# Kernel tuning notes

Measured on AMD Instinct MI355X. Metric: run time of the kernel, lower is better.

## Reference

```python
import jax, jax.numpy as jnp
import numpy as np

N, S, F, D = 4096, 128, 128, 256  # batch, memory slots, feat_dim, dim_h_o
EPS = 1e-8  # torch CosineSimilarity eps


def _xavier(key, shape):
    fan_out, fan_in = shape
    std = float(np.sqrt(2.0 / (fan_in + fan_out)))
    return jax.random.normal(key, shape, dtype=jnp.float32) * std


def setup_inputs() -> dict:
    key = jax.random.key(0)
    ks = jax.random.split(key, 10)
    return {
        "h_o_prev": jax.random.normal(ks[0], (N, D), dtype=jnp.float32),
        "C": jax.random.normal(ks[1], (N, S, F), dtype=jnp.float32),
        "Wk": _xavier(ks[2], (F, D)), "bk": jnp.zeros((F,), jnp.float32),
        "Wb": _xavier(ks[3], (1, D)), "bb": jnp.zeros((1,), jnp.float32),
        "We": _xavier(ks[4], (F, D)), "be": jnp.zeros((F,), jnp.float32),
        "Wv": _xavier(ks[5], (F, D)), "bv": jnp.zeros((F,), jnp.float32),
        "Wih": _xavier(ks[6], (3 * D, F)), "Whh": _xavier(ks[7], (3 * D, D)),
        "bih": jnp.zeros((3 * D,), jnp.float32), "bhh": jnp.zeros((3 * D,), jnp.float32),
    }


def reference(h_o_prev, C, Wk, bk, Wb, bb, We, be, Wv, bv, Wih, Whh, bih, bhh):
    # --- Attention (content addressing) ---
    k = h_o_prev @ Wk.T + bk                              # [N, F]
    beta_pre = h_o_prev @ Wb.T + bb                       # [N, 1]
    # clamp-split softplus trick in source == softplus(x) + 1
    beta = jax.nn.softplus(beta_pre) + 1.0                # [N, 1]
    C_norm = jnp.maximum(jnp.linalg.norm(C, axis=2), EPS)           # [N, S]
    k_norm = jnp.maximum(jnp.linalg.norm(k, axis=1, keepdims=True), EPS)  # [N, 1]
    s = jnp.einsum("nsf,nf->ns", C, k) / (C_norm * k_norm)          # cosine sim [N, S]
    w = jax.nn.softmax(s * beta, axis=1)                  # [N, S]
    # --- Read memory ---
    r = jnp.einsum("ns,nsf->nf", w, C)                    # [N, F]
    # --- GRU cell update (torch GRUCell semantics) ---
    gi = r @ Wih.T + bih                                  # [N, 3D]
    gh = h_o_prev @ Whh.T + bhh                           # [N, 3D]
    i_r, i_z, i_n = jnp.split(gi, 3, axis=1)
    h_r, h_z, h_n = jnp.split(gh, 3, axis=1)
    rg = jax.nn.sigmoid(i_r + h_r)
    z = jax.nn.sigmoid(i_z + h_z)
    n = jnp.tanh(i_n + rg * h_n)
    h_o = (1.0 - z) * n + z * h_o_prev                    # [N, D]
    # --- Write memory (erase + add, outer products) ---
    e = jax.nn.sigmoid(h_o @ We.T + be)                   # [N, F]
    v = h_o @ Wv.T + bv                                   # [N, F]
    w2 = w[:, :, None]                                    # [N, S, 1]
    C_new = C * (1.0 - w2 * e[:, None, :]) + w2 * v[:, None, :]
    return h_o, C_new, k, r
```

## Files before the change

### kernel.cpp

```cpp
#include <hip/hip_runtime.h>
#include <hip/hip_bf16.h>
#include <cstddef>
#include <cstdint>

constexpr int Nn = 4096;
constexpr int Ss = 128;
constexpr int Ff = 128;
constexpr int Dd = 256;
constexpr float EPSV = 1e-8f;

constexpr size_t HO_OFF = 0;
constexpr size_t C_OFF  = (size_t)Nn * Dd;
constexpr size_t K_OFF  = C_OFF + (size_t)Nn * Ss * Ff;
constexpr size_t R_OFF  = K_OFF + (size_t)Nn * Ff;

typedef __attribute__((ext_vector_type(4))) float f4v;
typedef __attribute__((ext_vector_type(8))) short bh8;

__device__ __forceinline__ float sigmf(float x) { return 1.0f / (1.0f + __expf(-x)); }

__device__ __forceinline__ short f2bf(float x) {
    __hip_bfloat16 h = __float2bfloat16(x);
    return *reinterpret_cast<short*>(&h);
}

template <int SIGSPLIT>
__global__ __launch_bounds__(256) void mfma_gemm(
    const float* __restrict__ A, int K,
    const float* __restrict__ W1, const float* __restrict__ W2, int splitW,
    const float* __restrict__ b1, const float* __restrict__ b2,
    float* __restrict__ out1, int J1,
    float* __restrict__ out2, int J2, int splitOut)
{
    __shared__ __align__(16) short sA[64 * 32];
    __shared__ __align__(16) short sW[64 * 32];

    const int t  = threadIdx.x;
    const int bm = blockIdx.x * 64;
    const int bj = blockIdx.y * 64;

    const int r  = t >> 2;
    const int kg = t & 3;
    const float* aRow = A + (size_t)(bm + r) * K;
    const int   colS  = bj + r;
    const float* wRow = (colS < splitW) ? (W1 + (size_t)colS * K)
                                        : (W2 + (size_t)(colS - splitW) * K);
    const int swzSt = r * 32 + ((kg ^ (r & 3)) << 3);

    const int l   = t & 63;
    const int wv  = t >> 6;
    const int wr  = wv >> 1;
    const int wc  = wv & 1;
    const int kgr = l >> 4;
    const int fr  = l & 15;

    f4v acc[2][2];
#pragma unroll
    for (int m = 0; m < 2; ++m)
#pragma unroll
        for (int n2 = 0; n2 < 2; ++n2) acc[m][n2] = f4v{0.f, 0.f, 0.f, 0.f};

    const int nk = K / 32;
    for (int kc = 0; kc < nk; ++kc) {
        const int k0 = kc * 32 + kg * 8;
        float4 a0 = *(const float4*)(aRow + k0);
        float4 a1 = *(const float4*)(aRow + k0 + 4);
        float4 w0 = *(const float4*)(wRow + k0);
        float4 w1 = *(const float4*)(wRow + k0 + 4);
        bh8 av = { f2bf(a0.x), f2bf(a0.y), f2bf(a0.z), f2bf(a0.w),
                   f2bf(a1.x), f2bf(a1.y), f2bf(a1.z), f2bf(a1.w) };
        bh8 wvv= { f2bf(w0.x), f2bf(w0.y), f2bf(w0.z), f2bf(w0.w),
                   f2bf(w1.x), f2bf(w1.y), f2bf(w1.z), f2bf(w1.w) };
        __syncthreads();
        *(bh8*)(sA + swzSt) = av;
        *(bh8*)(sW + swzSt) = wvv;
        __syncthreads();

        bh8 af[2], bf[2];
#pragma unroll
        for (int m = 0; m < 2; ++m) {
            int ar = wr * 32 + m * 16 + fr;
            af[m] = *(bh8*)(sA + ar * 32 + ((kgr ^ (ar & 3)) << 3));
            int bc = wc * 32 + m * 16 + fr;
            bf[m] = *(bh8*)(sW + bc * 32 + ((kgr ^ (bc & 3)) << 3));
        }
#pragma unroll
        for (int m = 0; m < 2; ++m)
#pragma unroll
            for (int n2 = 0; n2 < 2; ++n2)
                acc[m][n2] = __builtin_amdgcn_mfma_f32_16x16x32_bf16(
                    af[m], bf[n2], acc[m][n2], 0, 0, 0);
    }

#pragma unroll
    for (int n2 = 0; n2 < 2; ++n2) {
        const int colg = bj + wc * 32 + n2 * 16 + fr;
        const float bs = (colg < splitW) ? b1[colg] : b2[colg - splitW];
        float* base; int jj;
        if (colg < splitOut) { base = out1 + colg;              jj = J1; }
        else                 { base = out2 + (colg - splitOut); jj = J2; }
#pragma unroll
        for (int m = 0; m < 2; ++m) {
#pragma unroll
            for (int rg = 0; rg < 4; ++rg) {
                float x = acc[m][n2][rg] + bs;
                if (SIGSPLIT && colg < SIGSPLIT) x = sigmf(x);
                const int rowg = bm + wr * 32 + m * 16 + kgr * 4 + rg;
                base[(size_t)rowg * jj] = x;
            }
        }
    }
}

__global__ __launch_bounds__(256) void beta_kernel(
    const float* __restrict__ h, const float* __restrict__ Wb,
    const float* __restrict__ bb, float* __restrict__ beta_out)
{
    int wid  = threadIdx.x >> 6;
    int lane = threadIdx.x & 63;
    int n    = blockIdx.x * 4 + wid;
    float4 hv = *(const float4*)(h + (size_t)n * Dd + lane * 4);
    float4 wv = *(const float4*)(Wb + lane * 4);
    float p = hv.x * wv.x + hv.y * wv.y + hv.z * wv.z + hv.w * wv.w;
#pragma unroll
    for (int o = 32; o > 0; o >>= 1) p += __shfl_xor(p, o);
    if (lane == 0) {
        float bp = p + bb[0];
        float sp = (bp > 20.0f) ? bp : log1pf(__expf(bp));
        beta_out[n] = sp + 1.0f;
    }
}

__global__ __launch_bounds__(256) void attn_kernel(
    const float* __restrict__ C, const float* __restrict__ kvec,
    const float* __restrict__ beta_arr,
    float* __restrict__ w_out, float* __restrict__ r_out)
{
    const int n    = blockIdx.x;
    const int t    = threadIdx.x;
    const int lane = t & 63;
    const int wid  = t >> 6;
    const float* Cn = C + (size_t)n * Ss * Ff;

    __shared__ float sk[Ff];
    __shared__ float ssc[Ss];
    __shared__ float sred[8];
    __shared__ float sw[Ss];
    __shared__ float sr4[8][Ff];

    if (t < Ff) sk[t] = kvec[(size_t)n * Ff + t];
    __syncthreads();

    float ks = 0.0f;
    if (t < Ff) { float kv = sk[t]; ks = kv * kv; }
#pragma unroll
    for (int o = 32; o > 0; o >>= 1) ks += __shfl_xor(ks, o);
    if (lane == 0) sred[wid] = ks;
    __syncthreads();
    const float knorm = fmaxf(sqrtf(sred[0] + sred[1]), EPSV);
    const float beta  = beta_arr[n];

#pragma unroll 4
    for (int it = 0; it < 16; ++it) {
        int s = wid * 32 + it * 2 + (lane >> 5);
        int f = (lane & 31) * 4;
        float4 c4 = *(const float4*)(Cn + (size_t)s * Ff + f);
        float d = c4.x * sk[f] + c4.y * sk[f + 1] + c4.z * sk[f + 2] + c4.w * sk[f + 3];
        float q = c4.x * c4.x + c4.y * c4.y + c4.z * c4.z + c4.w * c4.w;
#pragma unroll
        for (int o = 16; o > 0; o >>= 1) {
            d += __shfl_xor(d, o);
            q += __shfl_xor(q, o);
        }
        if ((lane & 31) == 0) {
            float cn = fmaxf(sqrtf(q), EPSV);
            ssc[s] = d / (cn * knorm);
        }
    }
    __syncthreads();

    float x = -INFINITY;
    if (t < Ss) x = ssc[t] * beta;
    float m = x;
#pragma unroll
    for (int o = 32; o > 0; o >>= 1) m = fmaxf(m, __shfl_xor(m, o));
    if (lane == 0) sred[wid] = m;
    __syncthreads();
    const float gm = fmaxf(sred[0], sred[1]);
    float ex = (t < Ss) ? __expf(x - gm) : 0.0f;
    float sm = ex;
#pragma unroll
    for (int o = 32; o > 0; o >>= 1) sm += __shfl_xor(sm, o);
    if (lane == 0) sred[4 + wid] = sm;
    __syncthreads();
    const float tot = sred[4] + sred[5];
    if (t < Ss) {
        float wvl = ex / tot;
        sw[t] = wvl;
        w_out[(size_t)n * Ss + t] = wvl;
    }
    __syncthreads();

    const int f4 = (t & 31) * 4;
    const int sg = t >> 5;
    float4 racc = make_float4(0.f, 0.f, 0.f, 0.f);
#pragma unroll 4
    for (int j = 0; j < 16; ++j) {
        int s = sg * 16 + j;
        float wvl = sw[s];
        float4 c4 = *(const float4*)(Cn + (size_t)s * Ff + f4);
        racc.x += wvl * c4.x;
        racc.y += wvl * c4.y;
        racc.z += wvl * c4.z;
        racc.w += wvl * c4.w;
    }
    *(float4*)(&sr4[sg][f4]) = racc;
    __syncthreads();
    if (t < 32) {
        float4 rr = *(float4*)(&sr4[0][t * 4]);
#pragma unroll
        for (int g = 1; g < 8; ++g) {
            float4 p = *(float4*)(&sr4[g][t * 4]);
            rr.x += p.x; rr.y += p.y; rr.z += p.z; rr.w += p.w;
        }
        *(float4*)(r_out + (size_t)n * Ff + t * 4) = rr;
    }
}

__global__ __launch_bounds__(256) void gates_kernel(
    const float* __restrict__ gi, const float* __restrict__ gh,
    const float* __restrict__ hprev, float* __restrict__ ho)
{
    int idx = blockIdx.x * blockDim.x + threadIdx.x;
    int n  = idx >> 6;
    int d4 = (idx & 63) * 4;
    const float* gin = gi + (size_t)n * 768;
    const float* ghn = gh + (size_t)n * 768;
    float4 ir = *(const float4*)(gin + d4);
    float4 iz = *(const float4*)(gin + 256 + d4);
    float4 in_ = *(const float4*)(gin + 512 + d4);
    float4 hr = *(const float4*)(ghn + d4);
    float4 hz = *(const float4*)(ghn + 256 + d4);
    float4 hn = *(const float4*)(ghn + 512 + d4);
    float4 hp = *(const float4*)(hprev + (size_t)n * Dd + d4);
    float4 o;
    { float rg = sigmf(ir.x + hr.x); float z = sigmf(iz.x + hz.x);
      float nn = tanhf(in_.x + rg * hn.x); o.x = (1.0f - z) * nn + z * hp.x; }
    { float rg = sigmf(ir.y + hr.y); float z = sigmf(iz.y + hz.y);
      float nn = tanhf(in_.y + rg * hn.y); o.y = (1.0f - z) * nn + z * hp.y; }
    { float rg = sigmf(ir.z + hr.z); float z = sigmf(iz.z + hz.z);
      float nn = tanhf(in_.z + rg * hn.z); o.z = (1.0f - z) * nn + z * hp.z; }
    { float rg = sigmf(ir.w + hr.w); float z = sigmf(iz.w + hz.w);
      float nn = tanhf(in_.w + rg * hn.w); o.w = (1.0f - z) * nn + z * hp.w; }
    *(float4*)(ho + (size_t)n * Dd + d4) = o;
}

__global__ __launch_bounds__(256) void update_kernel(
    const float* __restrict__ C, const float* __restrict__ w,
    const float* __restrict__ ev, float* __restrict__ Cnew)
{
    const size_t total4 = (size_t)Nn * Ss * Ff / 4;
    const size_t stride = (size_t)gridDim.x * blockDim.x;
    const size_t lin    = (size_t)blockIdx.x * blockDim.x + threadIdx.x;
    const int nIter     = (int)(total4 / stride);
    for (int it = nIter - 1; it >= 0; --it) {
        size_t i = (size_t)it * stride + lin;
        int n   = (int)(i >> 12);
        int rem = (int)(i & 4095);
        int s   = rem >> 5;
        int f4  = (rem & 31) * 4;
        float wv = w[(size_t)n * Ss + s];
        float4 e4 = *(const float4*)(ev + (size_t)n * 256 + f4);
        float4 v4 = *(const float4*)(ev + (size_t)n * 256 + 128 + f4);
        f4v c4 = __builtin_nontemporal_load((const f4v*)(C + i * 4));
        f4v o;
        o.x = c4.x * (1.0f - wv * e4.x) + wv * v4.x;
        o.y = c4.y * (1.0f - wv * e4.y) + wv * v4.y;
        o.z = c4.z * (1.0f - wv * e4.z) + wv * v4.z;
        o.w = c4.w * (1.0f - wv * e4.w) + wv * v4.w;
        __builtin_nontemporal_store(o, (f4v*)(Cnew + i * 4));
    }
}

extern "C" void kernel_launch(void* const* d_in, const int* in_sizes, int n_in,
                              void* d_out, int out_size, void* d_ws, size_t ws_size,
                              hipStream_t stream)
{
    const float* h_prev = (const float*)d_in[0];
    const float* C      = (const float*)d_in[1];
    const float* Wk     = (const float*)d_in[2];
    const float* bk     = (const float*)d_in[3];
    const float* Wb     = (const float*)d_in[4];
    const float* bb     = (const float*)d_in[5];
    const float* We     = (const float*)d_in[6];
    const float* be     = (const float*)d_in[7];
    const float* Wv     = (const float*)d_in[8];
    const float* bv     = (const float*)d_in[9];
    const float* Wih    = (const float*)d_in[10];
    const float* Whh    = (const float*)d_in[11];
    const float* bih    = (const float*)d_in[12];
    const float* bhh    = (const float*)d_in[13];

    float* out  = (float*)d_out;
    float* ho   = out + HO_OFF;
    float* Cnew = out + C_OFF;
    float* kbuf = out + K_OFF;
    float* rbuf = out + R_OFF;

    float* ws      = (float*)d_ws;
    float* ws_gh   = ws;
    float* ws_gi   = ws_gh + (size_t)Nn * 768;
    float* ws_beta = ws_gi + (size_t)Nn * 768;
    float* ws_w    = ws_beta + Nn;
    float* ws_ev   = ws_w + (size_t)Nn * Ss;

    mfma_gemm<0><<<dim3(Nn / 64, 896 / 64), 256, 0, stream>>>(
        h_prev, Dd, Whh, Wk, 768, bhh, bk, ws_gh, 768, kbuf, 128, 768);

    beta_kernel<<<Nn / 4, 256, 0, stream>>>(h_prev, Wb, bb, ws_beta);

    attn_kernel<<<Nn, 256, 0, stream>>>(C, kbuf, ws_beta, ws_w, rbuf);

    mfma_gemm<0><<<dim3(Nn / 64, 768 / 64), 256, 0, stream>>>(
        rbuf, Ff, Wih, Wih, 768, bih, bih, ws_gi, 768, nullptr, 0, 768);

    gates_kernel<<<(Nn * Dd / 4) / 256, 256, 0, stream>>>(ws_gi, ws_gh, h_prev, ho);

    mfma_gemm<128><<<dim3(Nn / 64, 256 / 64), 256, 0, stream>>>(
        ho, Dd, We, Wv, 128, be, bv, ws_ev, 256, nullptr, 0, 256);

    update_kernel<<<8192, 256, 0, stream>>>(C, ws_w, ws_ev, Cnew);
}
```

Baseline: 227.8 us.

## Fuse whole memory-cell step into one per-batch-tile mega kernel

Replaces seven kernels with a weight-to-bf16 prep kernel and one fused kernel that handles 8 batch rows per block. Each block runs the key projection, the cosine attention with an online softmax, the GRU GEMMs and gates, and the erase/add GEMM and C update. Intermediates such as gi, gh, w and e/v stay in LDS, and C is read twice from the same block, which improves its chance of cache reuse. The cost is tiny MFMA tiles padded to 16 rows with only 8 used, fewer blocks in the grid, and heavy LDS use that may limit occupancy.

After: 191.0 us. 16.2% less time.

```diff
diff --git a/kernel.cpp b/kernel.cpp
--- a/kernel.cpp
+++ b/kernel.cpp
@@ -16,6 +16,13 @@
 
 typedef __attribute__((ext_vector_type(4))) float f4v;
 typedef __attribute__((ext_vector_type(8))) short bh8;
+typedef __attribute__((ext_vector_type(4))) short bh4;
+
+constexpr int WK_O  = 0;
+constexpr int WHH_O = 32768;
+constexpr int WIH_O = 229376;
+constexpr int WEV_O = 327680;
+constexpr int W_TOT = 393216;
 
 __device__ __forceinline__ float sigmf(float x) { return 1.0f / (1.0f + __expf(-x)); }
 
@@ -24,261 +31,248 @@
     return *reinterpret_cast<short*>(&h);
 }
 
-template <int SIGSPLIT>
-__global__ __launch_bounds__(256) void mfma_gemm(
-    const float* __restrict__ A, int K,
-    const float* __restrict__ W1, const float* __restrict__ W2, int splitW,
-    const float* __restrict__ b1, const float* __restrict__ b2,
-    float* __restrict__ out1, int J1,
-    float* __restrict__ out2, int J2, int splitOut)
+__device__ __forceinline__ int swzH(int row, int kb) { return row * 512 + (kb ^ ((row & 7) << 4)); }
+__device__ __forceinline__ int swzR(int row, int kb) { return row * 256 + (kb ^ ((row & 7) << 4)); }
+
+__device__ __forceinline__ f4v mfma16(bh8 a, bh8 b, f4v c) {
+    return __builtin_amdgcn_mfma_f32_16x16x32_bf16(a, b, c, 0, 0, 0);
+}
+
+__global__ __launch_bounds__(256) void prep_weights(
+    const float* __restrict__ Wk, const float* __restrict__ Whh,
+    const float* __restrict__ Wih, const float* __restrict__ We,
+    const float* __restrict__ Wv, short* __restrict__ out)
 {
-    __shared__ __align__(16) short sA[64 * 32];
-    __shared__ __align__(16) short sW[64 * 32];
+    int id = blockIdx.x * 256 + threadIdx.x;
+    float v;
+    if      (id < WHH_O) v = Wk[id - WK_O];
+    else if (id < WIH_O) v = Whh[id - WHH_O];
+    else if (id < WEV_O) v = Wih[id - WIH_O];
+    else if (id < WEV_O + 32768) v = We[id - WEV_O];
+    else v = Wv[id - WEV_O - 32768];
+    out[id] = f2bf(v);
+}
+
+__global__ __launch_bounds__(512, 4) void mega_kernel(
+    const float* __restrict__ C, const float* __restrict__ h_prev,
+    const short* __restrict__ WB,
+    const float* __restrict__ Wb, const float* __restrict__ bb,
+    const float* __restrict__ bk, const float* __restrict__ bhh,
+    const float* __restrict__ bih, const float* __restrict__ be,
+    const float* __restrict__ bv,
+    float* __restrict__ ho, float* __restrict__ Cnew,
+    float* __restrict__ kout, float* __restrict__ rout)
+{
+    __shared__ float sH[8][256];
+    __shared__ __align__(16) short sHb[16 * 256];
+    __shared__ __align__(16) short sRb[16 * 128];
+    __shared__ float sK[8][128];
+    __shared__ float sSc[8][128];
+    __shared__ float sGs[8][768];
+    __shared__ float sGn[8][256];
+    __shared__ float sEV[8][256];
 
     const int t  = threadIdx.x;
-    const int bm = blockIdx.x * 64;
-    const int bj = blockIdx.y * 64;
-
-    const int r  = t >> 2;
-    const int kg = t & 3;
-    const float* aRow = A + (size_t)(bm + r) * K;
-    const int   colS  = bj + r;
-    const float* wRow = (colS < splitW) ? (W1 + (size_t)colS * K)
-                                        : (W2 + (size_t)(colS - splitW) * K);
-    const int swzSt = r * 32 + ((kg ^ (r & 3)) << 3);
-
-    const int l   = t & 63;
-    const int wv  = t >> 6;
-    const int wr  = wv >> 1;
-    const int wc  = wv & 1;
-    const int kgr = l >> 4;
-    const int fr  = l & 15;
-
-    f4v acc[2][2];
-#pragma unroll
-    for (int m = 0; m < 2; ++m)
-#pragma unroll
-        for (int n2 = 0; n2 < 2; ++n2) acc[m][n2] = f4v{0.f, 0.f, 0.f, 0.f};
-
-    const int nk = K / 32;
-    for (int kc = 0; kc < nk; ++kc) {
-        const int k0 = kc * 32 + kg * 8;
-        float4 a0 = *(const float4*)(aRow + k0);
-        float4 a1 = *(const float4*)(aRow + k0 + 4);
-        float4 w0 = *(const float4*)(wRow + k0);
-        float4 w1 = *(const float4*)(wRow + k0 + 4);
-        bh8 av = { f2bf(a0.x), f2bf(a0.y), f2bf(a0.z), f2bf(a0.w),
-                   f2bf(a1.x), f2bf(a1.y), f2bf(a1.z), f2bf(a1.w) };
-        bh8 wvv= { f2bf(w0.x), f2bf(w0.y), f2bf(w0.z), f2bf(w0.w),
-                   f2bf(w1.x), f2bf(w1.y), f2bf(w1.z), f2bf(w1.w) };
-        __syncthreads();
-        *(bh8*)(sA + swzSt) = av;
-        *(bh8*)(sW + swzSt) = wvv;
-        __syncthreads();
-
-        bh8 af[2], bf[2];
-#pragma unroll
-        for (int m = 0; m < 2; ++m) {
-            int ar = wr * 32 + m * 16 + fr;
-            af[m] = *(bh8*)(sA + ar * 32 + ((kgr ^ (ar & 3)) << 3));
-            int bc = wc * 32 + m * 16 + fr;
-            bf[m] = *(bh8*)(sW + bc * 32 + ((kgr ^ (bc & 3)) << 3));
-        }
-#pragma unroll
-        for (int m = 0; m < 2; ++m)
-#pragma unroll
-            for (int n2 = 0; n2 < 2; ++n2)
-                acc[m][n2] = __builtin_amdgcn_mfma_f32_16x16x32_bf16(
-                    af[m], bf[n2], acc[m][n2], 0, 0, 0);
-    }
-
-#pragma unroll
-    for (int n2 = 0; n2 < 2; ++n2) {
-        const int colg = bj + wc * 32 + n2 * 16 + fr;
-        const float bs = (colg < splitW) ? b1[colg] : b2[colg - splitW];
-        float* base; int jj;
-        if (colg < splitOut) { base = out1 + colg;              jj = J1; }
-        else                 { base = out2 + (colg - splitOut); jj = J2; }
-#pragma unroll
-        for (int m = 0; m < 2; ++m) {
+    const int l  = t & 63;
+    const int wv = t >> 6;
+    const int nb = blockIdx.x * 8;
+    char* hb = (char*)sHb;
+    char* rb = (char*)sRb;
+
+    const short* WkB  = WB + WK_O;
+    const short* WhhB = WB + WHH_O;
+    const short* WihB = WB + WIH_O;
+    const short* WevB = WB + WEV_O;
+
+    {
+        const int f = t * 4, row = f >> 8, col = f & 255;
+        float4 hv = *(const float4*)(h_prev + (size_t)(nb + row) * Dd + col);
+        *(float4*)&sH[row][col] = hv;
+        bh4 hb4 = { f2bf(hv.x), f2bf(hv.y), f2bf(hv.z), f2bf(hv.w) };
+        *(bh4*)(hb + swzH(row, col * 2)) = hb4;
+        *(int4*)(hb + 8192 + t * 16) = int4{0, 0, 0, 0};
+        *(int*)(rb + 2048 + t * 4) = 0;
+    }
+    __syncthreads();
+
+    {
+        const int fr = l & 15, kq = l >> 4, rbase = kq * 4;
+        const int colg = wv * 16 + fr;
+        f4v acc = {0.f, 0.f, 0.f, 0.f};
+#pragma unroll
+        for (int kc = 0; kc < 8; ++kc) {
+            bh8 a = *(const bh8*)(hb + swzH(fr, kc * 64 + kq * 16));
+            bh8 b = *(const bh8*)(WkB + (size_t)colg * 256 + kc * 32 + kq * 8);
+            acc = mfma16(a, b, acc);
+        }
+        if (rbase < 8) {
+            const float bs = bk[colg];
 #pragma unroll
             for (int rg = 0; rg < 4; ++rg) {
-                float x = acc[m][n2][rg] + bs;
-                if (SIGSPLIT && colg < SIGSPLIT) x = sigmf(x);
-                const int rowg = bm + wr * 32 + m * 16 + kgr * 4 + rg;
-                base[(size_t)rowg * jj] = x;
-            }
-        }
-    }
-}
-
-__global__ __launch_bounds__(256) void beta_kernel(
-    const float* __restrict__ h, const float* __restrict__ Wb,
-    const float* __restrict__ bb, float* __restrict__ beta_out)
-{
-    int wid  = threadIdx.x >> 6;
-    int lane = threadIdx.x & 63;
-    int n    = blockIdx.x * 4 + wid;
-    float4 hv = *(const float4*)(h + (size_t)n * Dd + lane * 4);
-    float4 wv = *(const float4*)(Wb + lane * 4);
-    float p = hv.x * wv.x + hv.y * wv.y + hv.z * wv.z + hv.w * wv.w;
-#pragma unroll
-    for (int o = 32; o > 0; o >>= 1) p += __shfl_xor(p, o);
-    if (lane == 0) {
-        float bp = p + bb[0];
-        float sp = (bp > 20.0f) ? bp : log1pf(__expf(bp));
-        beta_out[n] = sp + 1.0f;
-    }
-}
-
-__global__ __launch_bounds__(256) void attn_kernel(
-    const float* __restrict__ C, const float* __restrict__ kvec,
-    const float* __restrict__ beta_arr,
-    float* __restrict__ w_out, float* __restrict__ r_out)
-{
-    const int n    = blockIdx.x;
-    const int t    = threadIdx.x;
-    const int lane = t & 63;
-    const int wid  = t >> 6;
-    const float* Cn = C + (size_t)n * Ss * Ff;
-
-    __shared__ float sk[Ff];
-    __shared__ float ssc[Ss];
-    __shared__ float sred[8];
-    __shared__ float sw[Ss];
-    __shared__ float sr4[8][Ff];
-
-    if (t < Ff) sk[t] = kvec[(size_t)n * Ff + t];
-    __syncthreads();
-
-    float ks = 0.0f;
-    if (t < Ff) { float kv = sk[t]; ks = kv * kv; }
-#pragma unroll
-    for (int o = 32; o > 0; o >>= 1) ks += __shfl_xor(ks, o);
-    if (lane == 0) sred[wid] = ks;
-    __syncthreads();
-    const float knorm = fmaxf(sqrtf(sred[0] + sred[1]), EPSV);
-    const float beta  = beta_arr[n];
-
+                float x = acc[rg] + bs;
+                sK[rbase + rg][colg] = x;
+                kout[(size_t)(nb + rbase + rg) * Ff + colg] = x;
+            }
+        }
+    }
+    __syncthreads();
+
+    float M_r = 0.0f, invL_r = 0.0f;
+    {
+        const int half = l >> 5, fl = l & 31, f4 = fl * 4;
+        const float* Cn = C + (size_t)(nb + wv) * (Ss * Ff);
+
+        float kv0 = sK[wv][l], kv1 = sK[wv][64 + l];
+        float ks = kv0 * kv0 + kv1 * kv1;
+#pragma unroll
+        for (int o = 32; o > 0; o >>= 1) ks += __shfl_xor(ks, o);
+        const float knorm = fmaxf(sqrtf(ks), EPSV);
+
+        float4 hv = *(const float4*)&sH[wv][l * 4];
+        float4 wb4 = *(const float4*)(Wb + l * 4);
+        float bp = hv.x * wb4.x + hv.y * wb4.y + hv.z * wb4.z + hv.w * wb4.w;
+#pragma unroll
+        for (int o = 32; o > 0; o >>= 1) bp += __shfl_xor(bp, o);
+        bp += bb[0];
+        const float beta = ((bp > 20.0f) ? bp : log1pf(__expf(bp))) + 1.0f;
+
+        const float4 kreg = *(const float4*)&sK[wv][f4];
+        float m = -INFINITY, lsum = 0.0f;
+        f4v racc = {0.f, 0.f, 0.f, 0.f};
 #pragma unroll 4
-    for (int it = 0; it < 16; ++it) {
-        int s = wid * 32 + it * 2 + (lane >> 5);
-        int f = (lane & 31) * 4;
-        float4 c4 = *(const float4*)(Cn + (size_t)s * Ff + f);
-        float d = c4.x * sk[f] + c4.y * sk[f + 1] + c4.z * sk[f + 2] + c4.w * sk[f + 3];
-        float q = c4.x * c4.x + c4.y * c4.y + c4.z * c4.z + c4.w * c4.w;
-#pragma unroll
-        for (int o = 16; o > 0; o >>= 1) {
-            d += __shfl_xor(d, o);
-            q += __shfl_xor(q, o);
-        }
-        if ((lane & 31) == 0) {
-            float cn = fmaxf(sqrtf(q), EPSV);
-            ssc[s] = d / (cn * knorm);
-        }
-    }
-    __syncthreads();
-
-    float x = -INFINITY;
-    if (t < Ss) x = ssc[t] * beta;
-    float m = x;
-#pragma unroll
-    for (int o = 32; o > 0; o >>= 1) m = fmaxf(m, __shfl_xor(m, o));
-    if (lane == 0) sred[wid] = m;
-    __syncthreads();
-    const float gm = fmaxf(sred[0], sred[1]);
-    float ex = (t < Ss) ? __expf(x - gm) : 0.0f;
-    float sm = ex;
-#pragma unroll
-    for (int o = 32; o > 0; o >>= 1) sm += __shfl_xor(sm, o);
-    if (lane == 0) sred[4 + wid] = sm;
-    __syncthreads();
-    const float tot = sred[4] + sred[5];
-    if (t < Ss) {
-        float wvl = ex / tot;
-        sw[t] = wvl;
-        w_out[(size_t)n * Ss + t] = wvl;
-    }
-    __syncthreads();
-
-    const int f4 = (t & 31) * 4;
-    const int sg = t >> 5;
-    float4 racc = make_float4(0.f, 0.f, 0.f, 0.f);
+        for (int it = 0; it < 64; ++it) {
+            const int s = it * 2 + half;
+            f4v c4 = *(const f4v*)(Cn + s * Ff + f4);
+            float d = c4.x * kreg.x + c4.y * kreg.y + c4.z * kreg.z + c4.w * kreg.w;
+            float q = c4.x * c4.x + c4.y * c4.y + c4.z * c4.z + c4.w * c4.w;
+#pragma unroll
+            for (int o = 16; o > 0; o >>= 1) { d += __shfl_xor(d, o); q += __shfl_xor(q, o); }
+            const float x = d / (fmaxf(sqrtf(q), EPSV) * knorm) * beta;
+            if (fl == 0) sSc[wv][s] = x;
+            const float mn   = fmaxf(m, x);
+            const float corr = __expf(m - mn);
+            const float p    = __expf(x - mn);
+            lsum = lsum * corr + p;
+            racc = racc * corr + p * c4;
+            m = mn;
+        }
+        float m2 = __shfl_xor(m, 32);
+        float l2 = __shfl_xor(lsum, 32);
+        f4v r2;
+        r2.x = __shfl_xor(racc.x, 32); r2.y = __shfl_xor(racc.y, 32);
+        r2.z = __shfl_xor(racc.z, 32); r2.w = __shfl_xor(racc.w, 32);
+        const float M  = fmaxf(m, m2);
+        const float e1 = __expf(m - M), e2 = __expf(m2 - M);
+        const float L  = lsum * e1 + l2 * e2;
+        const float iL = 1.0f / L;
+        f4v r4 = (racc * e1 + r2 * e2) * iL;
+        if (half == 0) {
+            *(f4v*)(rout + (size_t)(nb + wv) * Ff + f4) = r4;
+            bh4 rb4 = { f2bf(r4.x), f2bf(r4.y), f2bf(r4.z), f2bf(r4.w) };
+            *(bh4*)(rb + swzR(wv, f4 * 2)) = rb4;
+        }
+        M_r = M; invL_r = iL;
+    }
+    __syncthreads();
+
+    {
+        const int fr = l & 15, kq = l >> 4, rbase = kq * 4;
+#pragma unroll
+        for (int i = 0; i < 6; ++i) {
+            const int colg = i * 128 + wv * 16 + fr;
+            f4v aG = {0.f, 0.f, 0.f, 0.f}, aI = {0.f, 0.f, 0.f, 0.f};
+#pragma unroll
+            for (int kc = 0; kc < 8; ++kc) {
+                bh8 a = *(const bh8*)(hb + swzH(fr, kc * 64 + kq * 16));
+                bh8 b = *(const bh8*)(WhhB + (size_t)colg * 256 + kc * 32 + kq * 8);
+                aG = mfma16(a, b, aG);
+            }
+#pragma unroll
+            for (int kc = 0; kc < 4; ++kc) {
+                bh8 a = *(const bh8*)(rb + swzR(fr, kc * 64 + kq * 16));
+                bh8 b = *(const bh8*)(WihB + (size_t)colg * 128 + kc * 32 + kq * 8);
+                aI = mfma16(a, b, aI);
+            }
+            if (rbase < 8) {
+                if (colg < 512) {
+                    const float bs = bhh[colg] + bih[colg];
+#pragma unroll
+                    for (int rg = 0; rg < 4; ++rg)
+                        sGs[rbase + rg][colg] = aG[rg] + aI[rg] + bs;
+                } else {
+                    const float b1 = bhh[colg], b2 = bih[colg];
+#pragma unroll
+                    for (int rg = 0; rg < 4; ++rg) {
+                        sGs[rbase + rg][colg]       = aG[rg] + b1;
+                        sGn[rbase + rg][colg - 512] = aI[rg] + b2;
+                    }
+                }
+            }
+        }
+    }
+    __syncthreads();
+
+    {
+        const int d4 = l * 4;
+        float4 gr  = *(const float4*)&sGs[wv][d4];
+        float4 gz  = *(const float4*)&sGs[wv][256 + d4];
+        float4 hn  = *(const float4*)&sGs[wv][512 + d4];
+        float4 in_ = *(const float4*)&sGn[wv][d4];
+        float4 hp  = *(const float4*)&sH[wv][d4];
+        float4 o;
+        { float rg = sigmf(gr.x), z = sigmf(gz.x);
+          float nn = tanhf(in_.x + rg * hn.x); o.x = (1.0f - z) * nn + z * hp.x; }
+        { float rg = sigmf(gr.y), z = sigmf(gz.y);
+          float nn = tanhf(in_.y + rg * hn.y); o.y = (1.0f - z) * nn + z * hp.y; }
+        { float rg = sigmf(gr.z), z = sigmf(gz.z);
+          float nn = tanhf(in_.z + rg * hn.z); o.z = (1.0f - z) * nn + z * hp.z; }
+        { float rg = sigmf(gr.w), z = sigmf(gz.w);
+          float nn = tanhf(in_.w + rg * hn.w); o.w = (1.0f - z) * nn + z * hp.w; }
+        *(float4*)(ho + (size_t)(nb + wv) * Dd + d4) = o;
+        bh4 ob = { f2bf(o.x), f2bf(o.y), f2bf(o.z), f2bf(o.w) };
+        *(bh4*)(hb + swzH(wv, d4 * 2)) = ob;
+    }
+    __syncthreads();
+
+    {
+        const int fr = l & 15, kq = l >> 4, rbase = kq * 4;
+#pragma unroll
+        for (int i = 0; i < 2; ++i) {
+            const int colg = i * 128 + wv * 16 + fr;
+            f4v acc = {0.f, 0.f, 0.f, 0.f};
+#pragma unroll
+            for (int kc = 0; kc < 8; ++kc) {
+                bh8 a = *(const bh8*)(hb + swzH(fr, kc * 64 + kq * 16));
+                bh8 b = *(const bh8*)(WevB + (size_t)colg * 256 + kc * 32 + kq * 8);
+                acc = mfma16(a, b, acc);
+            }
+            if (rbase < 8) {
+                const float bs = (colg < 128) ? be[colg] : bv[colg - 128];
+#pragma unroll
+                for (int rg = 0; rg < 4; ++rg) {
+                    float x = acc[rg] + bs;
+                    if (colg < 128) x = sigmf(x);
+                    sEV[rbase + rg][colg] = x;
+                }
+            }
+        }
+    }
+    __syncthreads();
+
+    {
+        const int half = l >> 5, fl = l & 31, f4 = fl * 4;
+        const float* Cn = C    + (size_t)(nb + wv) * (Ss * Ff);
+        float*       Co = Cnew + (size_t)(nb + wv) * (Ss * Ff);
+        f4v e4 = *(const f4v*)&sEV[wv][f4];
+        f4v v4 = *(const f4v*)&sEV[wv][128 + f4];
 #pragma unroll 4
-    for (int j = 0; j < 16; ++j) {
-        int s = sg * 16 + j;
-        float wvl = sw[s];
-        float4 c4 = *(const float4*)(Cn + (size_t)s * Ff + f4);
-        racc.x += wvl * c4.x;
-        racc.y += wvl * c4.y;
-        racc.z += wvl * c4.z;
-        racc.w += wvl * c4.w;
-    }
-    *(float4*)(&sr4[sg][f4]) = racc;
-    __syncthreads();
-    if (t < 32) {
-        float4 rr = *(float4*)(&sr4[0][t * 4]);
-#pragma unroll
-        for (int g = 1; g < 8; ++g) {
-            float4 p = *(float4*)(&sr4[g][t * 4]);
-            rr.x += p.x; rr.y += p.y; rr.z += p.z; rr.w += p.w;
-        }
-        *(float4*)(r_out + (size_t)n * Ff + t * 4) = rr;
-    }
-}
-
-__global__ __launch_bounds__(256) void gates_kernel(
-    const float* __restrict__ gi, const float* __restrict__ gh,
-    const float* __restrict__ hprev, float* __restrict__ ho)
-{
-    int idx = blockIdx.x * blockDim.x + threadIdx.x;
-    int n  = idx >> 6;
-    int d4 = (idx & 63) * 4;
-    const float* gin = gi + (size_t)n * 768;
-    const float* ghn = gh + (size_t)n * 768;
-    float4 ir = *(const float4*)(gin + d4);
-    float4 iz = *(const float4*)(gin + 256 + d4);
-    float4 in_ = *(const float4*)(gin + 512 + d4);
-    float4 hr = *(const float4*)(ghn + d4);
-    float4 hz = *(const float4*)(ghn + 256 + d4);
-    float4 hn = *(const float4*)(ghn + 512 + d4);
-    float4 hp = *(const float4*)(hprev + (size_t)n * Dd + d4);
-    float4 o;
-    { float rg = sigmf(ir.x + hr.x); float z = sigmf(iz.x + hz.x);
-      float nn = tanhf(in_.x + rg * hn.x); o.x = (1.0f - z) * nn + z * hp.x; }
-    { float rg = sigmf(ir.y + hr.y); float z = sigmf(iz.y + hz.y);
-      float nn = tanhf(in_.y + rg * hn.y); o.y = (1.0f - z) * nn + z * hp.y; }
-    { float rg = sigmf(ir.z + hr.z); float z = sigmf(iz.z + hz.z);
-      float nn = tanhf(in_.z + rg * hn.z); o.z = (1.0f - z) * nn + z * hp.z; }
-    { float rg = sigmf(ir.w + hr.w); float z = sigmf(iz.w + hz.w);
-      float nn = tanhf(in_.w + rg * hn.w); o.w = (1.0f - z) * nn + z * hp.w; }
-    *(float4*)(ho + (size_t)n * Dd + d4) = o;
-}
-
-__global__ __launch_bounds__(256) void update_kernel(
-    const float* __restrict__ C, const float* __restrict__ w,
-    const float* __restrict__ ev, float* __restrict__ Cnew)
-{
-    const size_t total4 = (size_t)Nn * Ss * Ff / 4;
-    const size_t stride = (size_t)gridDim.x * blockDim.x;
-    const size_t lin    = (size_t)blockIdx.x * blockDim.x + threadIdx.x;
-    const int nIter     = (int)(total4 / stride);
-    for (int it = nIter - 1; it >= 0; --it) {
-        size_t i = (size_t)it * stride + lin;
-        int n   = (int)(i >> 12);
-        int rem = (int)(i & 4095);
-        int s   = rem >> 5;
-        int f4  = (rem & 31) * 4;
-        float wv = w[(size_t)n * Ss + s];
-        float4 e4 = *(const float4*)(ev + (size_t)n * 256 + f4);
-        float4 v4 = *(const float4*)(ev + (size_t)n * 256 + 128 + f4);
-        f4v c4 = __builtin_nontemporal_load((const f4v*)(C + i * 4));
-        f4v o;
-        o.x = c4.x * (1.0f - wv * e4.x) + wv * v4.x;
-        o.y = c4.y * (1.0f - wv * e4.y) + wv * v4.y;
-        o.z = c4.z * (1.0f - wv * e4.z) + wv * v4.z;
-        o.w = c4.w * (1.0f - wv * e4.w) + wv * v4.w;
-        __builtin_nontemporal_store(o, (f4v*)(Cnew + i * 4));
+        for (int it = 0; it < 64; ++it) {
+            const int s = it * 2 + half;
+            const float wsc = __expf(sSc[wv][s] - M_r) * invL_r;
+            f4v c4 = *(const f4v*)(Cn + s * Ff + f4);
+            f4v o = c4 * (1.0f - wsc * e4) + wsc * v4;
+            __builtin_nontemporal_store(o, (f4v*)(Co + s * Ff + f4));
+        }
     }
 }
 
@@ -307,27 +301,11 @@
     float* kbuf = out + K_OFF;
     float* rbuf = out + R_OFF;
 
-    float* ws      = (float*)d_ws;
-    float* ws_gh   = ws;
-    float* ws_gi   = ws_gh + (size_t)Nn * 768;
-    float* ws_beta = ws_gi + (size_t)Nn * 768;
-    float* ws_w    = ws_beta + Nn;
-    float* ws_ev   = ws_w + (size_t)Nn * Ss;
-
-    mfma_gemm<0><<<dim3(Nn / 64, 896 / 64), 256, 0, stream>>>(
-        h_prev, Dd, Whh, Wk, 768, bhh, bk, ws_gh, 768, kbuf, 128, 768);
-
-    beta_kernel<<<Nn / 4, 256, 0, stream>>>(h_prev, Wb, bb, ws_beta);
-
-    attn_kernel<<<Nn, 256, 0, stream>>>(C, kbuf, ws_beta, ws_w, rbuf);
-
-    mfma_gemm<0><<<dim3(Nn / 64, 768 / 64), 256, 0, stream>>>(
-        rbuf, Ff, Wih, Wih, 768, bih, bih, ws_gi, 768, nullptr, 0, 768);
-
-    gates_kernel<<<(Nn * Dd / 4) / 256, 256, 0, stream>>>(ws_gi, ws_gh, h_prev, ho);
-
-    mfma_gemm<128><<<dim3(Nn / 64, 256 / 64), 256, 0, stream>>>(
-        ho, Dd, We, Wv, 128, be, bv, ws_ev, 256, nullptr, 0, 256);
-
-    update_kernel<<<8192, 256, 0, stream>>>(C, ws_w, ws_ev, Cnew);
-}
+    short* wsB = (short*)d_ws;
+
+    prep_weights<<<W_TOT / 256, 256, 0, stream>>>(Wk, Whh, Wih, We, Wv, wsB);
+
+    mega_kernel<<<Nn / 8, 512, 0, stream>>>(
+        C, h_prev, wsB, Wb, bb, bk, bhh, bih, be, bv,
+        ho, Cnew, kbuf, rbuf);
+}
```
